# Kernel optimization log

Hardware: AMD Instinct MI355X
Metric: run time of the kernel (lower is better)

Reference implementation:

```python
import jax, jax.numpy as jnp
import numpy as np

B, C, H, W, K = 2, 36, 512, 512, 9
GROUPS, GSIZE = 3, 12  # channel groups 0:12, 12:24, 24:36


def _grid_sample_bilinear(feat, gx, gy):
    """Bilinear grid_sample, align_corners=True. feat [B,C,H,W]; gx,gy [B,H,W] in [-1,1]."""
    Bn, Cn, Hn, Wn = feat.shape
    px = (gx + 1.0) * 0.5 * (Wn - 1)
    py = (gy + 1.0) * 0.5 * (Hn - 1)
    x0 = jnp.floor(px)
    y0 = jnp.floor(py)
    wx = (px - x0)[:, None, :, :]
    wy = (py - y0)[:, None, :, :]
    x0i = jnp.clip(x0.astype(jnp.int32), 0, Wn - 1)
    x1i = jnp.clip(x0i + 1, 0, Wn - 1)
    y0i = jnp.clip(y0.astype(jnp.int32), 0, Hn - 1)
    y1i = jnpip = jnp.clip(y0.astype(jnp.int32) + 1, 0, Hn - 1)
    flat = feat.reshape(Bn, Cn, Hn * Wn)
    gather = jax.vmap(lambda f, yi, xi: f[:, yi * Wn + xi])  # -> [B,C,H,W]
    v00 = gather(flat, y0i, x0i)
    v01 = gather(flat, y0i, x1i)
    v10 = gather(flat, y1i, x0i)
    v11 = gather(flat, y1i, x1i)
    return (v00 * (1 - wx) * (1 - wy) + v01 * wx * (1 - wy)
            + v10 * (1 - wx) * wy + v11 * wx * wy)


def setup_inputs() -> dict:
    key = jax.random.key(0)
    k1, k2, k3 = jax.random.split(key, 3)
    features = jax.random.normal(k1, (B, C, H, W), jnp.float32)
    offset_x = jax.random.normal(k2, (B, K, H, W), jnp.float32) * 16.0
    offset_y = jax.random.normal(k3, (B, K, H, W), jnp.float32) * 16.0
    left_x = jnp.broadcast_to(jnp.arange(W, dtype=jnp.float32)[None, None, None, :], (B, 1, H, W))
    left_y = jnp.broadcast_to(jnp.arange(H, dtype=jnp.float32)[None, None, :, None], (B, 1, H, W))
    return {"features": features, "offset_x": offset_x, "offset_y": offset_y,
            "left_x": jnp.array(left_x), "left_y": jnp.array(left_y)}


def reference(features, offset_x, offset_y, left_x, left_y):
    Hn, Wn = features.shape[2], features.shape[3]
    # clamp candidate coords to image, then normalize to [-1,1]
    rx = jnp.clip(left_x + offset_x, 0.0, Wn - 1)
    ry = jnp.clip(left_y + offset_y, 0.0, Hn - 1)
    gx = (rx - (Wn - 1) / 2.0) / ((Wn - 1) / 2.0)  # [B,K,H,W]
    gy = (ry - (Hn - 1) / 2.0) / ((Hn - 1) / 2.0)

    def per_candidate(g):
        gxk, gyk = g  # each [B,H,W]
        a = _grid_sample_bilinear(features, gxk, gyk)  # [B,36,H,W]
        a2 = jnp.roll(a, 12, axis=1)
        a3 = jnp.roll(a, 24, axis=1)

        def grp_mean(d):  # [B,36,H,W] -> [B,3,H,W] mean over 12-channel groups
            return d.reshape(d.shape[0], GROUPS, GSIZE, d.shape[2], d.shape[3]).mean(axis=2)

        s = jnp.concatenate([grp_mean(-jnp.abs(features - a)),
                             grp_mean(-jnp.abs(features - a2)),
                             grp_mean(-jnp.abs(features - a3))], axis=1)  # [B,9,H,W]
        return jnp.max(s, axis=1)  # top-1 of sort == max  -> [B,H,W]

    strengths = jax.lax.map(per_candidate,
                            (jnp.moveaxis(gx, 1, 0), jnp.moveaxis(gy, 1, 0)))  # [K,B,H,W]
    strengths = jnp.moveaxis(strengths, 0, 1)  # [B,K,H,W]

    wgt = jax.nn.softmax(strengths * 1000.0, axis=1)
    ox = jnp.sum(offset_x * wgt, axis=1, keepdims=True)
    oy = jnp.sum(offset_y * wgt, axis=1, keepdims=True)
    oy = jnp.clip(oy + left_y, 0.0, Hn - 1) - left_y
    ox = jnp.clip(ox + left_x, 0.0, Wn - 1) - left_x
    return ox, oy
```

## Files before the change

kernel.cpp:

```cpp
#include <hip/hip_runtime.h>
#include <math.h>

#define B_ 2
#define C_ 36
#define H_ 512
#define W_ 512
#define K_ 9
#define HW_ (H_ * W_)
#define ROWF4 (W_ * C_ / 4)

__global__ __launch_bounds__(256) void transpose_kernel(const float* __restrict__ in,
                                                        float* __restrict__ out) {
  __shared__ float tile[64][37];
  int blk = blockIdx.x;
  int wt = blk & 7;
  int h = (blk >> 3) & (H_ - 1);
  int b = blk >> 12;
  int w0 = wt << 6;
  int tid = threadIdx.x;
  const float* src = in + ((size_t)b * C_) * HW_ + (size_t)h * W_ + w0;
#pragma unroll
  for (int it = 0; it < 9; ++it) {
    int idx = it * 256 + tid;
    int c = idx >> 6;
    int wl = idx & 63;
    tile[wl][c] = src[(size_t)c * HW_ + wl];
  }
  __syncthreads();
  float* dst = out + (((size_t)b * H_ + h) * W_ + w0) * C_;
#pragma unroll
  for (int it = 0; it < 9; ++it) {
    int idx = it * 256 + tid;
    int wl = idx / 36;
    int c = idx - wl * 36;
    dst[idx] = tile[wl][c];
  }
}

__global__ __launch_bounds__(64, 2) void eval_kernel_cw(const float* __restrict__ feat,
                                                        const float* __restrict__ offx,
                                                        const float* __restrict__ offy,
                                                        float* __restrict__ out) {
  __shared__ __align__(16) float scratch[64 * 36];
  __shared__ __align__(16) float4 w_lds[64];
  __shared__ int a_lds[64];

  int tid = threadIdx.x;
  int blk = blockIdx.x;
  int region = blk & 7;
  int slot = blk >> 3;
  int b = region >> 2;
  int qd = region & 3;
  int qy = (qd >> 1) << 8;
  int qx = (qd & 1) << 8;
  int tr = slot >> 5;
  int tc = slot & 31;
  if (tr & 1) tc = 31 - tc;
  int h = qy + tr * 8 + (tid >> 3);
  int w = qx + tc * 8 + (tid & 7);
  int ph = h * W_ + w;
  int p = b * HW_ + ph;

  const float4* feat4 = reinterpret_cast<const float4*>(feat);

  const float* oxb = offx + (size_t)b * K_ * HW_ + ph;
  const float* oyb = offy + (size_t)b * K_ * HW_ + ph;
  float oxv[K_], oyv[K_];
#pragma unroll
  for (int k = 0; k < K_; ++k) {
    oxv[k] = oxb[k * HW_];
    oyv[k] = oyb[k * HW_];
  }

  float F[C_];
  {
    const float4* myF = feat4 + (size_t)p * 9;
#pragma unroll
    for (int i = 0; i < 9; ++i) {
      float4 v = myF[i];
      F[4 * i + 0] = v.x; F[4 * i + 1] = v.y; F[4 * i + 2] = v.z; F[4 * i + 3] = v.w;
    }
  }

  int g = tid / 9;
  int q = tid - 9 * g;

  float lx = (float)w;
  float ly = (float)h;

  float M = -INFINITY, den = 0.f, axs = 0.f, ays = 0.f;

#pragma unroll 1
  for (int k = 0; k < K_; ++k) {
    float ox = oxv[k];
    float oy = oyv[k];
    float rx = fminf(fmaxf(lx + ox, 0.0f), 511.0f);
    float ry = fminf(fmaxf(ly + oy, 0.0f), 511.0f);
    float gx = (rx - 255.5f) / 255.5f;
    float gy = (ry - 255.5f) / 255.5f;
    float px = (gx + 1.0f) * 0.5f * 511.0f;
    float py = (gy + 1.0f) * 0.5f * 511.0f;
    int x0 = (int)floorf(px); x0 = (x0 > 510) ? 510 : x0;
    int y0 = (int)floorf(py); y0 = (y0 > 510) ? 510 : y0;
    float wx = px - (float)x0;
    float wy = py - (float)y0;
    w_lds[tid] = make_float4((1.0f - wx) * (1.0f - wy), wx * (1.0f - wy),
                             (1.0f - wx) * wy, wx * wy);
    a_lds[tid] = ((b * H_ + y0) * W_ + x0) * 9;
    __syncthreads();

    float4 L[5][4];
#pragma unroll
    for (int r = 0; r < 5; ++r) {
      int tt = 7 * r + g;
      int t = (tt > 63) ? 63 : tt;
      const float4* r0 = feat4 + a_lds[t];
      L[r][0] = r0[q];
      L[r][1] = r0[9 + q];
      L[r][2] = r0[ROWF4 + q];
      L[r][3] = r0[ROWF4 + 9 + q];
    }
#pragma unroll
    for (int r = 0; r < 10; ++r) {
      int s = r % 5;
      int tt = 7 * r + g;
      int t = (tt > 63) ? 63 : tt;
      float4 W4 = w_lds[t];
      float4 v00 = L[s][0], v01 = L[s][1], v10 = L[s][2], v11 = L[s][3];
      float4 a4;
      a4.x = W4.x * v00.x + W4.y * v01.x + W4.z * v10.x + W4.w * v11.x;
      a4.y = W4.x * v00.y + W4.y * v01.y + W4.z * v10.y + W4.w * v11.y;
      a4.z = W4.x * v00.z + W4.y * v01.z + W4.z * v10.z + W4.w * v11.z;
      a4.w = W4.x * v00.w + W4.y * v01.w + W4.z * v10.w + W4.w * v11.w;
      if (tt < 64 && tid < 63) {
        *reinterpret_cast<float4*>(&scratch[t * 36 + 4 * q]) = a4;
      }
      if (r + 5 < 10) {
        int tt2 = 7 * (r + 5) + g;
        int t2 = (tt2 > 63) ? 63 : tt2;
        const float4* r0 = feat4 + a_lds[t2];
        L[s][0] = r0[q];
        L[s][1] = r0[9 + q];
        L[s][2] = r0[ROWF4 + q];
        L[s][3] = r0[ROWF4 + 9 + q];
      }
    }
    __syncthreads();

    float D[9] = {0.f, 0.f, 0.f, 0.f, 0.f, 0.f, 0.f, 0.f, 0.f};
    const float4* sc = reinterpret_cast<const float4*>(&scratch[tid * 36]);
#pragma unroll
    for (int q2 = 0; q2 < 9; ++q2) {
      float4 a4 = sc[q2];
      float av[4] = {a4.x, a4.y, a4.z, a4.w};
      int ga = q2 / 3;
      int f0 = 4 * (q2 % 3);
#pragma unroll
      for (int j = 0; j < 4; ++j) {
        D[ga]     += fabsf(F[f0 + j]      - av[j]);
        D[3 + ga] += fabsf(F[12 + f0 + j] - av[j]);
        D[6 + ga] += fabsf(F[24 + f0 + j] - av[j]);
      }
    }
    float mn = D[0];
#pragma unroll
    for (int j = 1; j < 9; ++j) mn = fminf(mn, D[j]);
    float xk = -(mn / 12.0f) * 1000.0f;

    float nm = fmaxf(M, xk);
    float scl = expf(M - nm);
    float ek = expf(xk - nm);
    den = den * scl + ek;
    axs = axs * scl + ox * ek;
    ays = ays * scl + oy * ek;
    M = nm;
  }

  float resx = axs / den;
  float resy = ays / den;
  out[p] = fminf(fmaxf(resx + lx, 0.0f), 511.0f) - lx;
  out[B_ * HW_ + p] = fminf(fmaxf(resy + ly, 0.0f), 511.0f) - ly;
}

__global__ __launch_bounds__(256) void eval_kernel_n(const float* __restrict__ feat,
                                                     const float* __restrict__ offx,
                                                     const float* __restrict__ offy,
                                                     float* __restrict__ out) {
  int p = blockIdx.x * 256 + threadIdx.x;
  int ph = p & (HW_ - 1);
  int b = p >> 18;
  float F[C_];
  const float* fb = feat + (size_t)b * C_ * HW_ + ph;
#pragma unroll
  for (int c = 0; c < C_; ++c) F[c] = fb[(size_t)c * HW_];
  float lx = (float)(ph & (W_ - 1));
  float ly = (float)((ph >> 9) & (H_ - 1));
  const float* oxb = offx + (size_t)b * K_ * HW_ + ph;
  const float* oyb = offy + (size_t)b * K_ * HW_ + ph;
  float M = -INFINITY, den = 0.f, ax = 0.f, ay = 0.f;
#pragma unroll 1
  for (int k = 0; k < K_; ++k) {
    float ox = oxb[k * HW_];
    float oy = oyb[k * HW_];
    float rx = fminf(fmaxf(lx + ox, 0.0f), 511.0f);
    float ry = fminf(fmaxf(ly + oy, 0.0f), 511.0f);
    float gx = (rx - 255.5f) / 255.5f;
    float gy = (ry - 255.5f) / 255.5f;
    float px = (gx + 1.0f) * 0.5f * 511.0f;
    float py = (gy + 1.0f) * 0.5f * 511.0f;
    int x0 = (int)floorf(px); x0 = (x0 > 510) ? 510 : x0;
    int y0 = (int)floorf(py); y0 = (y0 > 510) ? 510 : y0;
    float wx = px - (float)x0;
    float wy = py - (float)y0;
    float w00 = (1.0f - wx) * (1.0f - wy);
    float w01 = wx * (1.0f - wy);
    float w10 = (1.0f - wx) * wy;
    float w11 = wx * wy;
    float D[9] = {0.f, 0.f, 0.f, 0.f, 0.f, 0.f, 0.f, 0.f, 0.f};
    const float* pl = feat + (size_t)b * C_ * HW_ + (size_t)y0 * W_ + x0;
#pragma unroll
    for (int c = 0; c < C_; ++c) {
      const float* q0 = pl + (size_t)c * HW_;
      float v00 = q0[0], v01 = q0[1];
      float v10 = q0[W_], v11 = q0[W_ + 1];
      float a = v00 * w00 + v01 * w01 + v10 * w10 + v11 * w11;
      int i = c % 12;
      int ga = c / 12;
      D[ga]     += fabsf(F[i]      - a);
      D[3 + ga] += fabsf(F[12 + i] - a);
      D[6 + ga] += fabsf(F[24 + i] - a);
    }
    float mn = D[0];
#pragma unroll
    for (int j = 1; j < 9; ++j) mn = fminf(mn, D[j]);
    float xk = -(mn / 12.0f) * 1000.0f;
    float nm = fmaxf(M, xk);
    float sc = expf(M - nm);
    float ek = expf(xk - nm);
    den = den * sc + ek;
    ax = ax * sc + ox * ek;
    ay = ay * sc + oy * ek;
    M = nm;
  }
  float resx = ax / den;
  float resy = ay / den;
  out[p] = fminf(fmaxf(resx + lx, 0.0f), 511.0f) - lx;
  out[B_ * HW_ + p] = fminf(fmaxf(resy + ly, 0.0f), 511.0f) - ly;
}

extern "C" void kernel_launch(void* const* d_in, const int* in_sizes, int n_in,
                              void* d_out, int out_size, void* d_ws, size_t ws_size,
                              hipStream_t stream) {
  const float* features = (const float*)d_in[0];
  const float* offset_x = (const float*)d_in[1];
  const float* offset_y = (const float*)d_in[2];
  float* out = (float*)d_out;

  const int npix = B_ * HW_;
  const size_t need = (size_t)npix * C_ * sizeof(float);

  if (ws_size >= need) {
    float* featT = (float*)d_ws;
    transpose_kernel<<<B_ * H_ * (W_ / 64), 256, 0, stream>>>(features, featT);
    eval_kernel_cw<<<npix / 64, 64, 0, stream>>>(featT, offset_x, offset_y, out);
  } else {
    eval_kernel_n<<<npix / 256, 256, 0, stream>>>(features, offset_x, offset_y, out);
  }
}
```

Measured before the change: 321.4 us.

## Split bilinear gather into two half-tiles and overlap loads with scoring

```diff
diff --git a/kernel.cpp b/kernel.cpp
--- a/kernel.cpp
+++ b/kernel.cpp
@@ -41,7 +41,7 @@
                                                         const float* __restrict__ offx,
                                                         const float* __restrict__ offy,
                                                         float* __restrict__ out) {
-  __shared__ __align__(16) float scratch[64 * 36];
+  __shared__ __align__(16) float scratch[32 * 36];
   __shared__ __align__(16) float4 w_lds[64];
   __shared__ int a_lds[64];
 
@@ -113,6 +113,31 @@
 #pragma unroll
     for (int r = 0; r < 5; ++r) {
       int tt = 7 * r + g;
+      int t = (tt > 31) ? 31 : tt;
+      const float4* r0 = feat4 + a_lds[t];
+      L[r][0] = r0[q];
+      L[r][1] = r0[9 + q];
+      L[r][2] = r0[ROWF4 + q];
+      L[r][3] = r0[ROWF4 + 9 + q];
+    }
+#pragma unroll
+    for (int r = 0; r < 5; ++r) {
+      int tt = 7 * r + g;
+      int t = (tt > 31) ? 31 : tt;
+      float4 W4 = w_lds[t];
+      float4 v00 = L[r][0], v01 = L[r][1], v10 = L[r][2], v11 = L[r][3];
+      float4 a4;
+      a4.x = W4.x * v00.x + W4.y * v01.x + W4.z * v10.x + W4.w * v11.x;
+      a4.y = W4.x * v00.y + W4.y * v01.y + W4.z * v10.y + W4.w * v11.y;
+      a4.z = W4.x * v00.z + W4.y * v01.z + W4.z * v10.z + W4.w * v11.z;
+      a4.w = W4.x * v00.w + W4.y * v01.w + W4.z * v10.w + W4.w * v11.w;
+      if (tt < 32 && tid < 63) {
+        *reinterpret_cast<float4*>(&scratch[t * 36 + 4 * q]) = a4;
+      }
+    }
+#pragma unroll
+    for (int r = 0; r < 5; ++r) {
+      int tt = 32 + 7 * r + g;
       int t = (tt > 63) ? 63 : tt;
       const float4* r0 = feat4 + a_lds[t];
       L[r][0] = r0[q];
@@ -120,60 +145,77 @@
       L[r][2] = r0[ROWF4 + q];
       L[r][3] = r0[ROWF4 + 9 + q];
     }
-#pragma unroll
-    for (int r = 0; r < 10; ++r) {
-      int s = r % 5;
-      int tt = 7 * r + g;
+    if (tid < 32) {
+      float D[9] = {0.f, 0.f, 0.f, 0.f, 0.f, 0.f, 0.f, 0.f, 0.f};
+      const float4* sc = reinterpret_cast<const float4*>(&scratch[tid * 36]);
+#pragma unroll
+      for (int q2 = 0; q2 < 9; ++q2) {
+        float4 a4 = sc[q2];
+        float av[4] = {a4.x, a4.y, a4.z, a4.w};
+        int ga = q2 / 3;
+        int f0 = 4 * (q2 % 3);
+#pragma unroll
+        for (int j = 0; j < 4; ++j) {
+          D[ga]     += fabsf(F[f0 + j]      - av[j]);
+          D[3 + ga] += fabsf(F[12 + f0 + j] - av[j]);
+          D[6 + ga] += fabsf(F[24 + f0 + j] - av[j]);
+        }
+      }
+      float mn = D[0];
+#pragma unroll
+      for (int j = 1; j < 9; ++j) mn = fminf(mn, D[j]);
+      float xk = -(mn / 12.0f) * 1000.0f;
+      float nm = fmaxf(M, xk);
+      float scl = expf(M - nm);
+      float ek = expf(xk - nm);
+      den = den * scl + ek;
+      axs = axs * scl + ox * ek;
+      ays = ays * scl + oy * ek;
+      M = nm;
+    }
+#pragma unroll
+    for (int r = 0; r < 5; ++r) {
+      int tt = 32 + 7 * r + g;
       int t = (tt > 63) ? 63 : tt;
       float4 W4 = w_lds[t];
-      float4 v00 = L[s][0], v01 = L[s][1], v10 = L[s][2], v11 = L[s][3];
+      float4 v00 = L[r][0], v01 = L[r][1], v10 = L[r][2], v11 = L[r][3];
       float4 a4;
       a4.x = W4.x * v00.x + W4.y * v01.x + W4.z * v10.x + W4.w * v11.x;
       a4.y = W4.x * v00.y + W4.y * v01.y + W4.z * v10.y + W4.w * v11.y;
       a4.z = W4.x * v00.z + W4.y * v01.z + W4.z * v10.z + W4.w * v11.z;
       a4.w = W4.x * v00.w + W4.y * v01.w + W4.z * v10.w + W4.w * v11.w;
       if (tt < 64 && tid < 63) {
-        *reinterpret_cast<float4*>(&scratch[t * 36 + 4 * q]) = a4;
+        *reinterpret_cast<float4*>(&scratch[(t - 32) * 36 + 4 * q]) = a4;
       }
-      if (r + 5 < 10) {
-        int tt2 = 7 * (r + 5) + g;
-        int t2 = (tt2 > 63) ? 63 : tt2;
-        const float4* r0 = feat4 + a_lds[t2];
-        L[s][0] = r0[q];
-        L[s][1] = r0[9 + q];
-        L[s][2] = r0[ROWF4 + q];
-        L[s][3] = r0[ROWF4 + 9 + q];
+    }
+    if (tid >= 32) {
+      float D[9] = {0.f, 0.f, 0.f, 0.f, 0.f, 0.f, 0.f, 0.f, 0.f};
+      const float4* sc = reinterpret_cast<const float4*>(&scratch[(tid - 32) * 36]);
+#pragma unroll
+      for (int q2 = 0; q2 < 9; ++q2) {
+        float4 a4 = sc[q2];
+        float av[4] = {a4.x, a4.y, a4.z, a4.w};
+        int ga = q2 / 3;
+        int f0 = 4 * (q2 % 3);
+#pragma unroll
+        for (int j = 0; j < 4; ++j) {
+          D[ga]     += fabsf(F[f0 + j]      - av[j]);
+          D[3 + ga] += fabsf(F[12 + f0 + j] - av[j]);
+          D[6 + ga] += fabsf(F[24 + f0 + j] - av[j]);
+        }
       }
-    }
-    __syncthreads();
-
-    float D[9] = {0.f, 0.f, 0.f, 0.f, 0.f, 0.f, 0.f, 0.f, 0.f};
-    const float4* sc = reinterpret_cast<const float4*>(&scratch[tid * 36]);
-#pragma unroll
-    for (int q2 = 0; q2 < 9; ++q2) {
-      float4 a4 = sc[q2];
-      float av[4] = {a4.x, a4.y, a4.z, a4.w};
-      int ga = q2 / 3;
-      int f0 = 4 * (q2 % 3);
-#pragma unroll
-      for (int j = 0; j < 4; ++j) {
-        D[ga]     += fabsf(F[f0 + j]      - av[j]);
-        D[3 + ga] += fabsf(F[12 + f0 + j] - av[j]);
-        D[6 + ga] += fabsf(F[24 + f0 + j] - av[j]);
-      }
-    }
-    float mn = D[0];
-#pragma unroll
-    for (int j = 1; j < 9; ++j) mn = fminf(mn, D[j]);
-    float xk = -(mn / 12.0f) * 1000.0f;
-
-    float nm = fmaxf(M, xk);
-    float scl = expf(M - nm);
-    float ek = expf(xk - nm);
-    den = den * scl + ek;
-    axs = axs * scl + ox * ek;
-    ays = ays * scl + oy * ek;
-    M = nm;
+      float mn = D[0];
+#pragma unroll
+      for (int j = 1; j < 9; ++j) mn = fminf(mn, D[j]);
+      float xk = -(mn / 12.0f) * 1000.0f;
+      float nm = fmaxf(M, xk);
+      float scl = expf(M - nm);
+      float ek = expf(xk - nm);
+      den = den * scl + ek;
+      axs = axs * scl + ox * ek;
+      ays = ays * scl + oy * ek;
+      M = nm;
+    }
   }
 
   float resx = axs / den;
```

Result: faster. 313.5 us (-2.5%).

## Replace LDS broadcast and block barriers with wave shuffles in 256-thread blocks

Applied to the files above, without the earlier changes.

```diff
diff --git a/kernel.cpp b/kernel.cpp
--- a/kernel.cpp
+++ b/kernel.cpp
@@ -37,15 +37,15 @@
   }
 }
 
-__global__ __launch_bounds__(64, 2) void eval_kernel_cw(const float* __restrict__ feat,
-                                                        const float* __restrict__ offx,
-                                                        const float* __restrict__ offy,
-                                                        float* __restrict__ out) {
-  __shared__ __align__(16) float scratch[64 * 36];
-  __shared__ __align__(16) float4 w_lds[64];
-  __shared__ int a_lds[64];
+__global__ __launch_bounds__(256, 3) void eval_kernel_cw(const float* __restrict__ feat,
+                                                         const float* __restrict__ offx,
+                                                         const float* __restrict__ offy,
+                                                         float* __restrict__ out) {
+  __shared__ __align__(16) float scratch[4][64 * 36];
 
   int tid = threadIdx.x;
+  int wv = tid >> 6;
+  int lane = tid & 63;
   int blk = blockIdx.x;
   int region = blk & 7;
   int slot = blk >> 3;
@@ -53,24 +53,21 @@
   int qd = region & 3;
   int qy = (qd >> 1) << 8;
   int qx = (qd & 1) << 8;
-  int tr = slot >> 5;
-  int tc = slot & 31;
-  if (tr & 1) tc = 31 - tc;
-  int h = qy + tr * 8 + (tid >> 3);
-  int w = qx + tc * 8 + (tid & 7);
+  int tr = slot >> 4;
+  int tc = slot & 15;
+  if (tr & 1) tc = 15 - tc;
+  int sy = (wv >> 1) << 3;
+  int sx = (wv & 1) << 3;
+  int h = qy + tr * 16 + sy + (lane >> 3);
+  int w = qx + tc * 16 + sx + (lane & 7);
   int ph = h * W_ + w;
   int p = b * HW_ + ph;
 
   const float4* feat4 = reinterpret_cast<const float4*>(feat);
+  float* scr = scratch[wv];
 
   const float* oxb = offx + (size_t)b * K_ * HW_ + ph;
   const float* oyb = offy + (size_t)b * K_ * HW_ + ph;
-  float oxv[K_], oyv[K_];
-#pragma unroll
-  for (int k = 0; k < K_; ++k) {
-    oxv[k] = oxb[k * HW_];
-    oyv[k] = oyb[k * HW_];
-  }
 
   float F[C_];
   {
@@ -82,18 +79,25 @@
     }
   }
 
-  int g = tid / 9;
-  int q = tid - 9 * g;
+  int g = lane / 9;
+  int q = lane - 9 * g;
 
   float lx = (float)w;
   float ly = (float)h;
 
   float M = -INFINITY, den = 0.f, axs = 0.f, ays = 0.f;
 
+  float oxc = oxb[0];
+  float oyc = oyb[0];
+
 #pragma unroll 1
   for (int k = 0; k < K_; ++k) {
-    float ox = oxv[k];
-    float oy = oyv[k];
+    float ox = oxc;
+    float oy = oyc;
+    if (k + 1 < K_) {
+      oxc = oxb[(k + 1) * HW_];
+      oyc = oyb[(k + 1) * HW_];
+    }
     float rx = fminf(fmaxf(lx + ox, 0.0f), 511.0f);
     float ry = fminf(fmaxf(ly + oy, 0.0f), 511.0f);
     float gx = (rx - 255.5f) / 255.5f;
@@ -104,17 +108,19 @@
     int y0 = (int)floorf(py); y0 = (y0 > 510) ? 510 : y0;
     float wx = px - (float)x0;
     float wy = py - (float)y0;
-    w_lds[tid] = make_float4((1.0f - wx) * (1.0f - wy), wx * (1.0f - wy),
-                             (1.0f - wx) * wy, wx * wy);
-    a_lds[tid] = ((b * H_ + y0) * W_ + x0) * 9;
-    __syncthreads();
+    float w00 = (1.0f - wx) * (1.0f - wy);
+    float w01 = wx * (1.0f - wy);
+    float w10 = (1.0f - wx) * wy;
+    float w11 = wx * wy;
+    int base = ((b * H_ + y0) * W_ + x0) * 9;
 
     float4 L[5][4];
 #pragma unroll
     for (int r = 0; r < 5; ++r) {
       int tt = 7 * r + g;
       int t = (tt > 63) ? 63 : tt;
-      const float4* r0 = feat4 + a_lds[t];
+      int bt = __shfl(base, t);
+      const float4* r0 = feat4 + bt;
       L[r][0] = r0[q];
       L[r][1] = r0[9 + q];
       L[r][2] = r0[ROWF4 + q];
@@ -125,30 +131,33 @@
       int s = r % 5;
       int tt = 7 * r + g;
       int t = (tt > 63) ? 63 : tt;
-      float4 W4 = w_lds[t];
+      float W00 = __shfl(w00, t);
+      float W01 = __shfl(w01, t);
+      float W10 = __shfl(w10, t);
+      float W11 = __shfl(w11, t);
       float4 v00 = L[s][0], v01 = L[s][1], v10 = L[s][2], v11 = L[s][3];
       float4 a4;
-      a4.x = W4.x * v00.x + W4.y * v01.x + W4.z * v10.x + W4.w * v11.x;
-      a4.y = W4.x * v00.y + W4.y * v01.y + W4.z * v10.y + W4.w * v11.y;
-      a4.z = W4.x * v00.z + W4.y * v01.z + W4.z * v10.z + W4.w * v11.z;
-      a4.w = W4.x * v00.w + W4.y * v01.w + W4.z * v10.w + W4.w * v11.w;
-      if (tt < 64 && tid < 63) {
-        *reinterpret_cast<float4*>(&scratch[t * 36 + 4 * q]) = a4;
+      a4.x = W00 * v00.x + W01 * v01.x + W10 * v10.x + W11 * v11.x;
+      a4.y = W00 * v00.y + W01 * v01.y + W10 * v10.y + W11 * v11.y;
+      a4.z = W00 * v00.z + W01 * v01.z + W10 * v10.z + W11 * v11.z;
+      a4.w = W00 * v00.w + W01 * v01.w + W10 * v10.w + W11 * v11.w;
+      if (tt < 64 && lane < 63) {
+        *reinterpret_cast<float4*>(&scr[t * 36 + 4 * q]) = a4;
       }
       if (r + 5 < 10) {
         int tt2 = 7 * (r + 5) + g;
         int t2 = (tt2 > 63) ? 63 : tt2;
-        const float4* r0 = feat4 + a_lds[t2];
+        int bt2 = __shfl(base, t2);
+        const float4* r0 = feat4 + bt2;
         L[s][0] = r0[q];
         L[s][1] = r0[9 + q];
         L[s][2] = r0[ROWF4 + q];
         L[s][3] = r0[ROWF4 + 9 + q];
       }
     }
-    __syncthreads();
 
     float D[9] = {0.f, 0.f, 0.f, 0.f, 0.f, 0.f, 0.f, 0.f, 0.f};
-    const float4* sc = reinterpret_cast<const float4*>(&scratch[tid * 36]);
+    const float4* sc = reinterpret_cast<const float4*>(&scr[lane * 36]);
 #pragma unroll
     for (int q2 = 0; q2 < 9; ++q2) {
       float4 a4 = sc[q2];
@@ -262,7 +271,7 @@
   if (ws_size >= need) {
     float* featT = (float*)d_ws;
     transpose_kernel<<<B_ * H_ * (W_ / 64), 256, 0, stream>>>(features, featT);
-    eval_kernel_cw<<<npix / 64, 64, 0, stream>>>(featT, offset_x, offset_y, out);
+    eval_kernel_cw<<<npix / 256, 256, 0, stream>>>(featT, offset_x, offset_y, out);
   } else {
     eval_kernel_n<<<npix / 256, 256, 0, stream>>>(features, offset_x, offset_y, out);
   }
```

New measurement: 325.0 us. Within noise of the previous version (+1.1%).
